# Optimization experiments

Hardware: AMD Instinct MI355X
Metric: run time of the kernel (lower is better)

The kernel has to match this reference:

```python
import jax, jax.numpy as jnp
import numpy as np

N_NODES = 50000
IN_CH = 64
REL_DIM = 32
N_EDGES = 800000
NEG_SLOPE = 0.01  # F.leaky_relu default


def _kgconv(x, src, dst, e, W, b, ai_w, ai_b, aj_w, aj_b, ew_w, ew_b):
    # x: [N, C]; src/dst: [E]; e: [E, C]
    x = x @ W.T + b
    x_i = x[dst]          # target node features  [E, C]
    x_j = x[src]          # source node features  [E, C]
    alpha = (x_i @ ai_w.T + ai_b) + (x_j @ aj_w.T + aj_b) + (e @ ew_w.T + ew_b)  # [E, 1]
    alpha = jax.nn.leaky_relu(alpha, NEG_SLOPE)
    # segment softmax keyed by edge_index[0] (source), as in the original code
    m = jax.ops.segment_max(alpha, src, num_segments=N_NODES)
    ex = jnp.exp(alpha - m[src])
    s = jax.ops.segment_sum(ex, src, num_segments=N_NODES)
    alpha = ex / (s[src] + 1e-16)
    msg = alpha * (x_j + e)                                  # [E, C]
    # PyG aggregates messages at target nodes (edge_index[1])
    out = jax.ops.segment_sum(msg, dst, num_segments=N_NODES)
    return jax.nn.relu(out)  # update()


def setup_inputs() -> dict:
    key = jax.random.key(0)
    ks = jax.random.split(key, 16)
    sc = 1.0 / np.sqrt(IN_CH)
    scr = 1.0 / np.sqrt(REL_DIM)
    def lin(k, out_d, in_d, s):
        k1, k2 = jax.random.split(k)
        return (jax.random.uniform(k1, (out_d, in_d), jnp.float32, -s, s),
                jax.random.uniform(k2, (out_d,), jnp.float32, -s, s))
    inp = {}
    inp["feat"] = jax.random.normal(ks[0], (N_NODES, IN_CH), jnp.float32)
    inp["edge_index"] = jax.random.randint(ks[1], (2, N_EDGES), 0, N_NODES)
    inp["r"] = jax.random.normal(ks[2], (N_EDGES, REL_DIM), jnp.float32)
    inp["rel_w"], inp["rel_b"] = lin(ks[3], IN_CH, REL_DIM, scr)
    for li, base in ((4, "c1"), (10, "c2")):
        inp[base + "_lin_w"], inp[base + "_lin_b"] = lin(ks[li], IN_CH, IN_CH, sc)
        inp[base + "_ai_w"], inp[base + "_ai_b"] = lin(ks[li + 1], 1, IN_CH, sc)
        inp[base + "_aj_w"], inp[base + "_aj_b"] = lin(ks[li + 2], 1, IN_CH, sc)
        inp[base + "_ew_w"], inp[base + "_ew_b"] = lin(ks[li + 3], 1, IN_CH, sc)
    return inp


def reference(feat, edge_index, r, rel_w, rel_b,
              c1_lin_w, c1_lin_b, c1_ai_w, c1_ai_b, c1_aj_w, c1_aj_b, c1_ew_w, c1_ew_b,
              c2_lin_w, c2_lin_b, c2_ai_w, c2_ai_b, c2_aj_w, c2_aj_b, c2_ew_w, c2_ew_b):
    src, dst = edge_index[0], edge_index[1]
    e = r @ rel_w.T + rel_b                                   # [E, IN_CH]
    x = _kgconv(feat, src, dst, e, c1_lin_w, c1_lin_b, c1_ai_w, c1_ai_b,
                c1_aj_w, c1_aj_b, c1_ew_w, c1_ew_b)
    x = jax.nn.relu(x)
    x = _kgconv(x, src, dst, e, c2_lin_w, c2_lin_b, c2_ai_w, c2_ai_b,
                c2_aj_w, c2_aj_b, c2_ew_w, c2_ew_b)
    return x
```

## Files before the change

kernel.cpp:

```cpp
#include <hip/hip_runtime.h>
#include <hip/hip_bf16.h>

using bf16 = __hip_bfloat16;

#define NEG_SLOPE 0.01f

__device__ __forceinline__ float bf_lo(unsigned int v) { return __uint_as_float(v << 16); }
__device__ __forceinline__ float bf_hi(unsigned int v) { return __uint_as_float(v & 0xffff0000u); }
__device__ __forceinline__ float b2f(unsigned short u) { return __uint_as_float((unsigned int)u << 16); }

__global__ void k_zero(unsigned int* __restrict__ p, int n) {
  int i = blockIdx.x * 256 + threadIdx.x;
  if (i < n) p[i] = 0u;
}

__global__ void k_prep(const float* __restrict__ rel_w, const float* __restrict__ rel_b,
                       const float* __restrict__ ew1_w, const float* __restrict__ ew1_b,
                       const float* __restrict__ ew2_w, const float* __restrict__ ew2_b,
                       const float* __restrict__ ai1_b, const float* __restrict__ aj1_b,
                       const float* __restrict__ ai2_b, const float* __restrict__ aj2_b,
                       float* __restrict__ consts) {
  int t = threadIdx.x;
  if (t < 32) {
    float a1 = 0.f, a2 = 0.f;
    for (int o = 0; o < 64; ++o) {
      float w = rel_w[o * 32 + t];
      a1 += w * ew1_w[o];
      a2 += w * ew2_w[o];
    }
    consts[t] = a1;
    consts[32 + t] = a2;
  } else if (t == 32) {
    float c = 0.f;
    for (int o = 0; o < 64; ++o) c += rel_b[o] * ew1_w[o];
    consts[64] = c + ew1_b[0] + ai1_b[0] + aj1_b[0];
  } else if (t == 33) {
    float c = 0.f;
    for (int o = 0; o < 64; ++o) c += rel_b[o] * ew2_w[o];
    consts[65] = c + ew2_b[0] + ai2_b[0] + aj2_b[0];
  }
}

__global__ void k_deg(const int* __restrict__ dst, int* __restrict__ deg, int E) {
  int e4 = (blockIdx.x * 256 + threadIdx.x) * 4;
  if (e4 + 3 < E) {
    int4 d = *(const int4*)(dst + e4);
    atomicAdd(&deg[d.x], 1);
    atomicAdd(&deg[d.y], 1);
    atomicAdd(&deg[d.z], 1);
    atomicAdd(&deg[d.w], 1);
  } else {
    for (int e = e4; e < E; ++e) atomicAdd(&deg[dst[e]], 1);
  }
}

__global__ __launch_bounds__(256) void k_scan_sum(const int* __restrict__ deg,
                                                  int* __restrict__ bsum, int N) {
  __shared__ int ws_[4];
  int t = threadIdx.x;
  int i = blockIdx.x * 256 + t;
  int v = (i < N) ? deg[i] : 0;
  #pragma unroll
  for (int m = 32; m >= 1; m >>= 1) v += __shfl_xor(v, m, 64);
  if ((t & 63) == 0) ws_[t >> 6] = v;
  __syncthreads();
  if (t == 0) bsum[blockIdx.x] = ws_[0] + ws_[1] + ws_[2] + ws_[3];
}

__global__ __launch_bounds__(256) void k_scan_bsum(const int* __restrict__ bsum,
                                                   int* __restrict__ bsumx,
                                                   int* __restrict__ off,
                                                   int NB, int N, int E) {
  __shared__ int part[256];
  int t = threadIdx.x;
  part[t] = (t < NB) ? bsum[t] : 0;
  __syncthreads();
  for (int d = 1; d < 256; d <<= 1) {
    int v = (t >= d) ? part[t - d] : 0;
    __syncthreads();
    part[t] += v;
    __syncthreads();
  }
  if (t < NB) bsumx[t] = (t == 0) ? 0 : part[t - 1];
  if (t == 0) off[N] = E;
}

__global__ __launch_bounds__(256) void k_scan_out(const int* __restrict__ deg,
                                                  const int* __restrict__ bsumx,
                                                  int* __restrict__ off,
                                                  int* __restrict__ pos, int N) {
  __shared__ int wsum[4];
  int t = threadIdx.x;
  int lane = t & 63;
  int wave = t >> 6;
  int i = blockIdx.x * 256 + t;
  int v = (i < N) ? deg[i] : 0;
  int incl = v;
  #pragma unroll
  for (int d = 1; d < 64; d <<= 1) {
    int u = __shfl_up(incl, d, 64);
    if (lane >= d) incl += u;
  }
  int wtot = __shfl(incl, 63, 64);
  if (lane == 0) wsum[wave] = wtot;
  __syncthreads();
  int woff = 0;
  for (int w = 0; w < 4; ++w) woff += (w < wave) ? wsum[w] : 0;
  if (i < N) {
    int o = bsumx[blockIdx.x] + woff + (incl - v);
    off[i] = o;
    pos[i] = o;
  }
}

__global__ void k_fill(const int* __restrict__ src, const int* __restrict__ dst,
                       int* __restrict__ pos, int* __restrict__ eid_s,
                       unsigned short* __restrict__ src_s,
                       unsigned short* __restrict__ dst_s, int E) {
  int e = blockIdx.x * 256 + threadIdx.x;
  if (e >= E) return;
  int d = dst[e];
  int p = atomicAdd(&pos[d], 1);
  eid_s[p] = e;
  src_s[p] = (unsigned short)src[e];
  dst_s[p] = (unsigned short)d;
}

__global__ __launch_bounds__(256) void k_perm(const int* __restrict__ eid_s,
                                              const float* __restrict__ r,
                                              const float* __restrict__ consts,
                                              float* __restrict__ ewd1_s,
                                              float* __restrict__ ewd2_s,
                                              bf16* __restrict__ r_s, int E) {
  int t = threadIdx.x;
  int k = t & 31;
  int g = blockIdx.x * 8 + (t >> 5);
  int p0 = g * 8;
  if (p0 >= E) return;
  float v1k = consts[k], v2k = consts[32 + k];
  float c1 = consts[64], c2 = consts[65];
  if (p0 + 8 <= E) {
    int e0 = eid_s[p0],     e1 = eid_s[p0 + 1], e2 = eid_s[p0 + 2], e3 = eid_s[p0 + 3];
    int e4 = eid_s[p0 + 4], e5 = eid_s[p0 + 5], e6 = eid_s[p0 + 6], e7 = eid_s[p0 + 7];
    float r0 = r[(size_t)e0 * 32 + k];
    float r1 = r[(size_t)e1 * 32 + k];
    float r2 = r[(size_t)e2 * 32 + k];
    float r3 = r[(size_t)e3 * 32 + k];
    float r4 = r[(size_t)e4 * 32 + k];
    float r5 = r[(size_t)e5 * 32 + k];
    float r6 = r[(size_t)e6 * 32 + k];
    float r7 = r[(size_t)e7 * 32 + k];
    bf16* wp = r_s + (size_t)p0 * 32 + k;
    wp[0]   = __float2bfloat16(r0);
    wp[32]  = __float2bfloat16(r1);
    wp[64]  = __float2bfloat16(r2);
    wp[96]  = __float2bfloat16(r3);
    wp[128] = __float2bfloat16(r4);
    wp[160] = __float2bfloat16(r5);
    wp[192] = __float2bfloat16(r6);
    wp[224] = __float2bfloat16(r7);
    float a0 = r0 * v1k, b0 = r0 * v2k;
    float a1 = r1 * v1k, b1 = r1 * v2k;
    float a2 = r2 * v1k, b2 = r2 * v2k;
    float a3 = r3 * v1k, b3 = r3 * v2k;
    float a4 = r4 * v1k, b4 = r4 * v2k;
    float a5 = r5 * v1k, b5 = r5 * v2k;
    float a6 = r6 * v1k, b6 = r6 * v2k;
    float a7 = r7 * v1k, b7 = r7 * v2k;
    #pragma unroll
    for (int m = 16; m >= 1; m >>= 1) {
      a0 += __shfl_xor(a0, m, 64);  b0 += __shfl_xor(b0, m, 64);
      a1 += __shfl_xor(a1, m, 64);  b1 += __shfl_xor(b1, m, 64);
      a2 += __shfl_xor(a2, m, 64);  b2 += __shfl_xor(b2, m, 64);
      a3 += __shfl_xor(a3, m, 64);  b3 += __shfl_xor(b3, m, 64);
      a4 += __shfl_xor(a4, m, 64);  b4 += __shfl_xor(b4, m, 64);
      a5 += __shfl_xor(a5, m, 64);  b5 += __shfl_xor(b5, m, 64);
      a6 += __shfl_xor(a6, m, 64);  b6 += __shfl_xor(b6, m, 64);
      a7 += __shfl_xor(a7, m, 64);  b7 += __shfl_xor(b7, m, 64);
    }
    if (k == 0) {
      ewd1_s[p0]     = a0 + c1;  ewd2_s[p0]     = b0 + c2;
      ewd1_s[p0 + 1] = a1 + c1;  ewd2_s[p0 + 1] = b1 + c2;
      ewd1_s[p0 + 2] = a2 + c1;  ewd2_s[p0 + 2] = b2 + c2;
      ewd1_s[p0 + 3] = a3 + c1;  ewd2_s[p0 + 3] = b3 + c2;
      ewd1_s[p0 + 4] = a4 + c1;  ewd2_s[p0 + 4] = b4 + c2;
      ewd1_s[p0 + 5] = a5 + c1;  ewd2_s[p0 + 5] = b5 + c2;
      ewd1_s[p0 + 6] = a6 + c1;  ewd2_s[p0 + 6] = b6 + c2;
      ewd1_s[p0 + 7] = a7 + c1;  ewd2_s[p0 + 7] = b7 + c2;
    }
  } else {
    for (int p = p0; p < E; ++p) {
      int e = eid_s[p];
      float rv = r[(size_t)e * 32 + k];
      r_s[(size_t)p * 32 + k] = __float2bfloat16(rv);
      float a = rv * v1k, b = rv * v2k;
      #pragma unroll
      for (int m = 16; m >= 1; m >>= 1) {
        a += __shfl_xor(a, m, 64);
        b += __shfl_xor(b, m, 64);
      }
      if (k == 0) { ewd1_s[p] = a + c1; ewd2_s[p] = b + c2; }
    }
  }
}

__global__ __launch_bounds__(256) void k_x(const float* __restrict__ in,
                                           const float* __restrict__ W,
                                           const float* __restrict__ b,
                                           const float* __restrict__ ai_w,
                                           const float* __restrict__ aj_w,
                                           bf16* __restrict__ x,
                                           float* __restrict__ aid,
                                           float* __restrict__ ajd, int N) {
  __shared__ float WT[64 * 64];
  int t = threadIdx.x;
  for (int idx = t; idx < 4096; idx += 256) {
    int o = idx >> 6, c = idx & 63;
    WT[c * 64 + o] = W[idx];
  }
  __syncthreads();
  int l = t & 63;
  int wave = t >> 6;
  int nwaves = gridDim.x * 4;
  float aw = ai_w[l], jw = aj_w[l], bl = b[l];
  for (int n = blockIdx.x * 4 + wave; n < N; n += nwaves) {
    float xin = in[(size_t)n * 64 + l];
    float acc = bl;
    #pragma unroll
    for (int c = 0; c < 64; ++c) {
      float bc = __shfl(xin, c, 64);
      acc += bc * WT[c * 64 + l];
    }
    x[(size_t)n * 64 + l] = __float2bfloat16(acc);
    float pa = acc * aw, pj = acc * jw;
    #pragma unroll
    for (int m = 32; m >= 1; m >>= 1) {
      pa += __shfl_xor(pa, m, 64);
      pj += __shfl_xor(pj, m, 64);
    }
    if (l == 0) { aid[n] = pa; ajd[n] = pj; }
  }
}

__global__ void k_alpha(const unsigned short* __restrict__ src_s,
                        const unsigned short* __restrict__ dst_s,
                        const float* __restrict__ aid, const float* __restrict__ ajd,
                        const float* __restrict__ ewd,
                        float* __restrict__ ex, float* __restrict__ s, int E) {
  int p4 = (blockIdx.x * 256 + threadIdx.x) * 4;
  if (p4 + 4 <= E) {
    ushort4 sv = *(const ushort4*)(src_s + p4);
    ushort4 dv = *(const ushort4*)(dst_s + p4);
    float4 ew = *(const float4*)(ewd + p4);
    float a0 = aid[dv.x] + ajd[sv.x] + ew.x;
    float a1 = aid[dv.y] + ajd[sv.y] + ew.y;
    float a2 = aid[dv.z] + ajd[sv.z] + ew.z;
    float a3 = aid[dv.w] + ajd[sv.w] + ew.w;
    a0 = (a0 > 0.f) ? a0 : a0 * NEG_SLOPE;
    a1 = (a1 > 0.f) ? a1 : a1 * NEG_SLOPE;
    a2 = (a2 > 0.f) ? a2 : a2 * NEG_SLOPE;
    a3 = (a3 > 0.f) ? a3 : a3 * NEG_SLOPE;
    float e0 = __expf(a0), e1 = __expf(a1), e2 = __expf(a2), e3 = __expf(a3);
    *(float4*)(ex + p4) = make_float4(e0, e1, e2, e3);
    atomicAdd(&s[sv.x], e0);
    atomicAdd(&s[sv.y], e1);
    atomicAdd(&s[sv.z], e2);
    atomicAdd(&s[sv.w], e3);
  } else if (p4 < E) {
    for (int p = p4; p < E; ++p) {
      int sn = src_s[p];
      float a = aid[dst_s[p]] + ajd[sn] + ewd[p];
      a = (a > 0.f) ? a : a * NEG_SLOPE;
      float ev = __expf(a);
      ex[p] = ev;
      atomicAdd(&s[sn], ev);
    }
  }
}

__global__ __launch_bounds__(256) void k_agg(const int* __restrict__ off,
                                             const unsigned short* __restrict__ src_s,
                                             const float* __restrict__ ex,
                                             const float* __restrict__ s,
                                             const bf16* __restrict__ x,
                                             const bf16* __restrict__ r_s,
                                             const float* __restrict__ rel_w,
                                             const float* __restrict__ rel_b,
                                             float* __restrict__ out, int N) {
  __shared__ float RT[32 * 64];
  int t = threadIdx.x;
  for (int idx = t; idx < 2048; idx += 256) {
    int o = idx >> 5, kk = idx & 31;
    RT[kk * 64 + o] = rel_w[idx];
  }
  __syncthreads();
  int l = t & 63;
  int k = l & 31;
  int half = l >> 5;
  int wave = t >> 6;
  int nwaves = gridDim.x * 4;
  const unsigned short* xu = (const unsigned short*)x;
  const unsigned short* ru = (const unsigned short*)r_s;
  float2 rbl = *(const float2*)(rel_b + 2 * k);
  for (int n = blockIdx.x * 4 + wave; n < N; n += nwaves) {
    int p0 = off[n], p1 = off[n + 1];
    float ax0 = 0.f, ax1 = 0.f, aq = 0.f, ws = 0.f;
    int b = p0;
    for (; b + 8 <= p1; b += 8) {
      int q0 = b + half, q1 = q0 + 2, q2 = q0 + 4, q3 = q0 + 6;
      int s0 = src_s[q0], s1 = src_s[q1], s2 = src_s[q2], s3 = src_s[q3];
      float w0 = ex[q0] * __builtin_amdgcn_rcpf(s[s0] + 1e-16f);
      float w1 = ex[q1] * __builtin_amdgcn_rcpf(s[s1] + 1e-16f);
      float w2 = ex[q2] * __builtin_amdgcn_rcpf(s[s2] + 1e-16f);
      float w3 = ex[q3] * __builtin_amdgcn_rcpf(s[s3] + 1e-16f);
      unsigned int xv0 = *(const unsigned int*)(xu + ((size_t)s0 << 6) + 2 * k);
      unsigned int xv1 = *(const unsigned int*)(xu + ((size_t)s1 << 6) + 2 * k);
      unsigned int xv2 = *(const unsigned int*)(xu + ((size_t)s2 << 6) + 2 * k);
      unsigned int xv3 = *(const unsigned int*)(xu + ((size_t)s3 << 6) + 2 * k);
      float rv0 = b2f(ru[(size_t)q0 * 32 + k]);
      float rv1 = b2f(ru[(size_t)q1 * 32 + k]);
      float rv2 = b2f(ru[(size_t)q2 * 32 + k]);
      float rv3 = b2f(ru[(size_t)q3 * 32 + k]);
      ax0 += w0 * bf_lo(xv0) + w1 * bf_lo(xv1) + w2 * bf_lo(xv2) + w3 * bf_lo(xv3);
      ax1 += w0 * bf_hi(xv0) + w1 * bf_hi(xv1) + w2 * bf_hi(xv2) + w3 * bf_hi(xv3);
      aq  += w0 * rv0 + w1 * rv1 + w2 * rv2 + w3 * rv3;
      ws  += w0 + w1 + w2 + w3;
    }
    for (; b + 2 <= p1; b += 2) {
      int q = b + half;
      int sn = src_s[q];
      float w = ex[q] * __builtin_amdgcn_rcpf(s[sn] + 1e-16f);
      unsigned int xv = *(const unsigned int*)(xu + ((size_t)sn << 6) + 2 * k);
      ax0 += w * bf_lo(xv);
      ax1 += w * bf_hi(xv);
      aq  += w * b2f(ru[(size_t)q * 32 + k]);
      ws  += w;
    }
    if (b < p1 && half == 0) {
      int sn = src_s[b];
      float w = ex[b] * __builtin_amdgcn_rcpf(s[sn] + 1e-16f);
      unsigned int xv = *(const unsigned int*)(xu + ((size_t)sn << 6) + 2 * k);
      ax0 += w * bf_lo(xv);
      ax1 += w * bf_hi(xv);
      aq  += w * b2f(ru[(size_t)b * 32 + k]);
      ws  += w;
    }
    ax0 += __shfl_xor(ax0, 32, 64);
    ax1 += __shfl_xor(ax1, 32, 64);
    aq  += __shfl_xor(aq, 32, 64);
    ws  += __shfl_xor(ws, 32, 64);
    float a0 = ax0 + ws * rbl.x;
    float a1 = ax1 + ws * rbl.y;
    #pragma unroll
    for (int kk = 0; kk < 32; ++kk) {
      float qk = __shfl(aq, kk, 32);
      float2 rt = *(const float2*)(RT + kk * 64 + 2 * k);
      a0 += qk * rt.x;
      a1 += qk * rt.y;
    }
    if (half == 0) {
      *(float2*)(out + ((size_t)n << 6) + 2 * k) =
          make_float2(fmaxf(a0, 0.f), fmaxf(a1, 0.f));
    }
  }
}

extern "C" void kernel_launch(void* const* d_in, const int* in_sizes, int n_in,
                              void* d_out, int out_size, void* d_ws, size_t ws_size,
                              hipStream_t stream) {
  const float* feat   = (const float*)d_in[0];
  const int*   eidx   = (const int*)d_in[1];
  const float* r      = (const float*)d_in[2];
  const float* rel_w  = (const float*)d_in[3];
  const float* rel_b  = (const float*)d_in[4];
  const float* c1_lw  = (const float*)d_in[5];
  const float* c1_lb  = (const float*)d_in[6];
  const float* c1_aiw = (const float*)d_in[7];
  const float* c1_aib = (const float*)d_in[8];
  const float* c1_ajw = (const float*)d_in[9];
  const float* c1_ajb = (const float*)d_in[10];
  const float* c1_eww = (const float*)d_in[11];
  const float* c1_ewb = (const float*)d_in[12];
  const float* c2_lw  = (const float*)d_in[13];
  const float* c2_lb  = (const float*)d_in[14];
  const float* c2_aiw = (const float*)d_in[15];
  const float* c2_aib = (const float*)d_in[16];
  const float* c2_ajw = (const float*)d_in[17];
  const float* c2_ajb = (const float*)d_in[18];
  const float* c2_eww = (const float*)d_in[19];
  const float* c2_ewb = (const float*)d_in[20];
  float* out = (float*)d_out;

  const int N = in_sizes[0] / 64;
  const int E = in_sizes[1] / 2;
  const int* src = eidx;
  const int* dst = eidx + E;

  float* wsf    = (float*)d_ws;
  float* consts = wsf;
  float* ewd1_s = wsf + 128;
  float* ewd2_s = ewd1_s + E;
  float* ex     = ewd2_s + E;
  float* s1     = ex + E;
  float* s2     = s1 + N;
  int*   deg    = (int*)(s2 + N);
  float* aid    = (float*)(deg + N);
  float* ajd    = aid + N;
  float* h1     = ajd + N;
  bf16*  x      = (bf16*)(h1 + (size_t)N * 64);
  int*   off    = (int*)(x + (size_t)N * 64);
  int*   pos    = off + N + 1;
  int*   bsum   = pos + N;
  int*   bsumx  = bsum + 256;
  size_t ofs = (size_t)((char*)(bsumx + 256) - (char*)d_ws);
  ofs = (ofs + 15) & ~(size_t)15;
  int* eid_s = (int*)((char*)d_ws + ofs);
  unsigned short* src_s = (unsigned short*)(eid_s + E);
  unsigned short* dst_s = src_s + E;
  bf16* r_s = (bf16*)(dst_s + E);

  const int blocksE   = (E + 255) / 256;
  const int blocksE4  = (E + 1023) / 1024;
  const int blocksP8  = (E + 63) / 64;
  const int blocksN   = (N + 255) / 256;
  const int blocksN3  = (3 * N + 255) / 256;
  const int gridP     = 2048;

  k_zero<<<blocksN3, 256, 0, stream>>>((unsigned int*)s1, 3 * N);
  k_prep<<<1, 64, 0, stream>>>(rel_w, rel_b, c1_eww, c1_ewb, c2_eww, c2_ewb,
                               c1_aib, c1_ajb, c2_aib, c2_ajb, consts);
  k_deg<<<blocksE4, 256, 0, stream>>>(dst, deg, E);
  k_scan_sum<<<blocksN, 256, 0, stream>>>(deg, bsum, N);
  k_scan_bsum<<<1, 256, 0, stream>>>(bsum, bsumx, off, blocksN, N, E);
  k_scan_out<<<blocksN, 256, 0, stream>>>(deg, bsumx, off, pos, N);
  k_fill<<<blocksE, 256, 0, stream>>>(src, dst, pos, eid_s, src_s, dst_s, E);
  k_perm<<<blocksP8, 256, 0, stream>>>(eid_s, r, consts, ewd1_s, ewd2_s, r_s, E);

  k_x<<<gridP, 256, 0, stream>>>(feat, c1_lw, c1_lb, c1_aiw, c1_ajw, x, aid, ajd, N);
  k_alpha<<<blocksE4, 256, 0, stream>>>(src_s, dst_s, aid, ajd, ewd1_s, ex, s1, E);
  k_agg<<<gridP, 256, 0, stream>>>(off, src_s, ex, s1, x, r_s, rel_w, rel_b, h1, N);

  k_x<<<gridP, 256, 0, stream>>>(h1, c2_lw, c2_lb, c2_aiw, c2_ajw, x, aid, ajd, N);
  k_alpha<<<blocksE4, 256, 0, stream>>>(src_s, dst_s, aid, ajd, ewd2_s, ex, s2, E);
  k_agg<<<gridP, 256, 0, stream>>>(off, src_s, ex, s2, x, r_s, rel_w, rel_b, out, N);
}
```

Before: 654.7 us.

## Pack edge id/src/dst into one 64-bit scatter and keep weights in registers

k_fill now writes a single packed 64-bit word per edge (edge id, dst, src) instead of three scattered stores. k_perm unpacks it, then writes src_s/dst_s as coalesced vector stores. k_x drops the shared-memory transposed weight matrix: each lane holds its 64-weight row in registers and reads the input row through uniform loads instead of 64 shuffles. The aim is fewer random scatter writes and less shuffle/LDS traffic, at the cost of 64 extra registers per thread in k_x and an extra read pass in k_perm.

```diff
diff --git a/kernel.cpp b/kernel.cpp
--- a/kernel.cpp
+++ b/kernel.cpp
@@ -114,23 +114,23 @@
 }
 
 __global__ void k_fill(const int* __restrict__ src, const int* __restrict__ dst,
-                       int* __restrict__ pos, int* __restrict__ eid_s,
-                       unsigned short* __restrict__ src_s,
-                       unsigned short* __restrict__ dst_s, int E) {
+                       int* __restrict__ pos, unsigned long long* __restrict__ ed,
+                       int E) {
   int e = blockIdx.x * 256 + threadIdx.x;
   if (e >= E) return;
   int d = dst[e];
   int p = atomicAdd(&pos[d], 1);
-  eid_s[p] = e;
-  src_s[p] = (unsigned short)src[e];
-  dst_s[p] = (unsigned short)d;
-}
-
-__global__ __launch_bounds__(256) void k_perm(const int* __restrict__ eid_s,
+  ed[p] = ((unsigned long long)(unsigned)e << 32) |
+          ((unsigned)d << 16) | (unsigned)src[e];
+}
+
+__global__ __launch_bounds__(256) void k_perm(const unsigned long long* __restrict__ ed,
                                               const float* __restrict__ r,
                                               const float* __restrict__ consts,
                                               float* __restrict__ ewd1_s,
                                               float* __restrict__ ewd2_s,
+                                              unsigned short* __restrict__ src_s,
+                                              unsigned short* __restrict__ dst_s,
                                               bf16* __restrict__ r_s, int E) {
   int t = threadIdx.x;
   int k = t & 31;
@@ -140,8 +140,10 @@
   float v1k = consts[k], v2k = consts[32 + k];
   float c1 = consts[64], c2 = consts[65];
   if (p0 + 8 <= E) {
-    int e0 = eid_s[p0],     e1 = eid_s[p0 + 1], e2 = eid_s[p0 + 2], e3 = eid_s[p0 + 3];
-    int e4 = eid_s[p0 + 4], e5 = eid_s[p0 + 5], e6 = eid_s[p0 + 6], e7 = eid_s[p0 + 7];
+    unsigned long long v0 = ed[p0],     v1 = ed[p0 + 1], v2 = ed[p0 + 2], v3 = ed[p0 + 3];
+    unsigned long long v4 = ed[p0 + 4], v5 = ed[p0 + 5], v6 = ed[p0 + 6], v7 = ed[p0 + 7];
+    int e0 = (int)(v0 >> 32), e1 = (int)(v1 >> 32), e2 = (int)(v2 >> 32), e3 = (int)(v3 >> 32);
+    int e4 = (int)(v4 >> 32), e5 = (int)(v5 >> 32), e6 = (int)(v6 >> 32), e7 = (int)(v7 >> 32);
     float r0 = r[(size_t)e0 * 32 + k];
     float r1 = r[(size_t)e1 * 32 + k];
     float r2 = r[(size_t)e2 * 32 + k];
@@ -187,10 +189,24 @@
       ewd1_s[p0 + 5] = a5 + c1;  ewd2_s[p0 + 5] = b5 + c2;
       ewd1_s[p0 + 6] = a6 + c1;  ewd2_s[p0 + 6] = b6 + c2;
       ewd1_s[p0 + 7] = a7 + c1;  ewd2_s[p0 + 7] = b7 + c2;
+      ushort4 sl, sh, dl, dh;
+      sl.x = (unsigned short)(v0 & 0xFFFF); sl.y = (unsigned short)(v1 & 0xFFFF);
+      sl.z = (unsigned short)(v2 & 0xFFFF); sl.w = (unsigned short)(v3 & 0xFFFF);
+      sh.x = (unsigned short)(v4 & 0xFFFF); sh.y = (unsigned short)(v5 & 0xFFFF);
+      sh.z = (unsigned short)(v6 & 0xFFFF); sh.w = (unsigned short)(v7 & 0xFFFF);
+      dl.x = (unsigned short)((v0 >> 16) & 0xFFFF); dl.y = (unsigned short)((v1 >> 16) & 0xFFFF);
+      dl.z = (unsigned short)((v2 >> 16) & 0xFFFF); dl.w = (unsigned short)((v3 >> 16) & 0xFFFF);
+      dh.x = (unsigned short)((v4 >> 16) & 0xFFFF); dh.y = (unsigned short)((v5 >> 16) & 0xFFFF);
+      dh.z = (unsigned short)((v6 >> 16) & 0xFFFF); dh.w = (unsigned short)((v7 >> 16) & 0xFFFF);
+      *(ushort4*)(src_s + p0)     = sl;
+      *(ushort4*)(src_s + p0 + 4) = sh;
+      *(ushort4*)(dst_s + p0)     = dl;
+      *(ushort4*)(dst_s + p0 + 4) = dh;
     }
   } else {
     for (int p = p0; p < E; ++p) {
-      int e = eid_s[p];
+      unsigned long long v = ed[p];
+      int e = (int)(v >> 32);
       float rv = r[(size_t)e * 32 + k];
       r_s[(size_t)p * 32 + k] = __float2bfloat16(rv);
       float a = rv * v1k, b = rv * v2k;
@@ -199,7 +215,11 @@
         a += __shfl_xor(a, m, 64);
         b += __shfl_xor(b, m, 64);
       }
-      if (k == 0) { ewd1_s[p] = a + c1; ewd2_s[p] = b + c2; }
+      if (k == 0) {
+        ewd1_s[p] = a + c1; ewd2_s[p] = b + c2;
+        src_s[p] = (unsigned short)(v & 0xFFFF);
+        dst_s[p] = (unsigned short)((v >> 16) & 0xFFFF);
+      }
     }
   }
 }
@@ -212,25 +232,31 @@
                                            bf16* __restrict__ x,
                                            float* __restrict__ aid,
                                            float* __restrict__ ajd, int N) {
-  __shared__ float WT[64 * 64];
-  int t = threadIdx.x;
-  for (int idx = t; idx < 4096; idx += 256) {
-    int o = idx >> 6, c = idx & 63;
-    WT[c * 64 + o] = W[idx];
-  }
-  __syncthreads();
+  int t = threadIdx.x;
   int l = t & 63;
-  int wave = t >> 6;
+  float w[64];
+  #pragma unroll
+  for (int c4 = 0; c4 < 16; ++c4) {
+    float4 v = *(const float4*)(W + l * 64 + c4 * 4);
+    w[c4 * 4]     = v.x;
+    w[c4 * 4 + 1] = v.y;
+    w[c4 * 4 + 2] = v.z;
+    w[c4 * 4 + 3] = v.w;
+  }
+  float aw = ai_w[l], jw = aj_w[l], bl = b[l];
+  int wid = __builtin_amdgcn_readfirstlane(t >> 6);
   int nwaves = gridDim.x * 4;
-  float aw = ai_w[l], jw = aj_w[l], bl = b[l];
-  for (int n = blockIdx.x * 4 + wave; n < N; n += nwaves) {
-    float xin = in[(size_t)n * 64 + l];
-    float acc = bl;
+  for (int n = blockIdx.x * 4 + wid; n < N; n += nwaves) {
+    const float* rowp = in + (size_t)n * 64;
+    float a0 = 0.f, a1 = 0.f, a2 = 0.f, a3 = 0.f;
     #pragma unroll
-    for (int c = 0; c < 64; ++c) {
-      float bc = __shfl(xin, c, 64);
-      acc += bc * WT[c * 64 + l];
-    }
+    for (int c = 0; c < 64; c += 4) {
+      a0 = fmaf(rowp[c],     w[c],     a0);
+      a1 = fmaf(rowp[c + 1], w[c + 1], a1);
+      a2 = fmaf(rowp[c + 2], w[c + 2], a2);
+      a3 = fmaf(rowp[c + 3], w[c + 3], a3);
+    }
+    float acc = bl + ((a0 + a1) + (a2 + a3));
     x[(size_t)n * 64 + l] = __float2bfloat16(acc);
     float pa = acc * aw, pj = acc * jw;
     #pragma unroll
@@ -414,8 +440,8 @@
   int*   bsumx  = bsum + 256;
   size_t ofs = (size_t)((char*)(bsumx + 256) - (char*)d_ws);
   ofs = (ofs + 15) & ~(size_t)15;
-  int* eid_s = (int*)((char*)d_ws + ofs);
-  unsigned short* src_s = (unsigned short*)(eid_s + E);
+  unsigned long long* ed = (unsigned long long*)((char*)d_ws + ofs);
+  unsigned short* src_s = (unsigned short*)(ed + E);
   unsigned short* dst_s = src_s + E;
   bf16* r_s = (bf16*)(dst_s + E);
 
@@ -433,8 +459,9 @@
   k_scan_sum<<<blocksN, 256, 0, stream>>>(deg, bsum, N);
   k_scan_bsum<<<1, 256, 0, stream>>>(bsum, bsumx, off, blocksN, N, E);
   k_scan_out<<<blocksN, 256, 0, stream>>>(deg, bsumx, off, pos, N);
-  k_fill<<<blocksE, 256, 0, stream>>>(src, dst, pos, eid_s, src_s, dst_s, E);
-  k_perm<<<blocksP8, 256, 0, stream>>>(eid_s, r, consts, ewd1_s, ewd2_s, r_s, E);
+  k_fill<<<blocksE, 256, 0, stream>>>(src, dst, pos, ed, E);
+  k_perm<<<blocksP8, 256, 0, stream>>>(ed, r, consts, ewd1_s, ewd2_s,
+                                       src_s, dst_s, r_s, E);
 
   k_x<<<gridP, 256, 0, stream>>>(feat, c1_lw, c1_lb, c1_aiw, c1_ajw, x, aid, ajd, N);
   k_alpha<<<blocksE4, 256, 0, stream>>>(src_s, dst_s, aid, ajd, ewd1_s, ex, s1, E);
```

Measured after the change: 606.3 us. 1.08x faster.
